# Optimization experiments

Measured on AMD Instinct MI355X. Metric: run time of the kernel, lower is better.

Reference implementation:

```python
import jax, jax.numpy as jnp
import numpy as np

B = 32768; E = 9; RANK = 50; K = 2
N_ENT = 40943; N_REL = 22
LOSS_COEF = 0.01; NOISE_EPS = 0.01
EPS = float(np.finfo(np.float64).eps)


def setup_inputs():
    key = jax.random.key(0)
    ks = jax.random.split(key, 12)
    q0 = jax.random.randint(ks[0], (B,), 0, N_ENT)
    q1 = jax.random.randint(ks[1], (B,), 0, N_REL)
    q2 = jax.random.randint(ks[2], (B,), 0, N_ENT)
    queries = jnp.stack([q0, q1, q2], axis=1)
    t2 = jax.random.randint(ks[3], (B,), 0, N_ENT)
    these_queries = jnp.stack([q0, q1, t2], axis=1)
    D = E * RANK
    entity = jax.random.normal(ks[4], (N_ENT, D), jnp.float32) / D
    rel = jax.random.normal(ks[5], (N_REL, 2 * D), jnp.float32) / (2 * D)
    rel_diag = 2.0 * jax.random.uniform(ks[6], (N_REL, D), jnp.float32) - 1.0
    bh = jnp.zeros((N_ENT, 1), jnp.float32)
    bt = jnp.zeros((N_ENT, 1), jnp.float32)
    c_param = jnp.ones((N_REL, 1), jnp.float32)
    cnn_w = 0.1 * jax.random.normal(ks[7], (1, 1, 5, 5), jnp.float32)
    cnn_b = jnp.zeros((1,), jnp.float32)
    h2e_w = 0.05 * jax.random.normal(ks[8], (E, 128), jnp.float32)
    h2e_b = jnp.zeros((E,), jnp.float32)
    cnnn_w = 0.1 * jax.random.normal(ks[9], (1, 1, 5, 5), jnp.float32)
    cnnn_b = jnp.zeros((1,), jnp.float32)
    h2en_w = 0.05 * jax.random.normal(ks[10], (E, 128), jnp.float32)
    h2en_b = jnp.zeros((E,), jnp.float32)
    noise = jax.random.normal(ks[11], (B, E), jnp.float32)
    return {"queries": queries, "these_queries": these_queries, "entity": entity,
            "rel": rel, "rel_diag": rel_diag, "bh": bh, "bt": bt, "c_param": c_param,
            "cnn_w": cnn_w, "cnn_b": cnn_b, "h2e_w": h2e_w, "h2e_b": h2e_b,
            "cnnn_w": cnnn_w, "cnnn_b": cnnn_b, "h2en_w": h2en_w, "h2en_b": h2en_b,
            "noise": noise}


def _conv(x, w, b):
    # x: [B,1,27,50], w: [1,1,5,5], stride 3, VALID -> [B,1,8,16]
    y = jax.lax.conv_general_dilated(x, w, (3, 3), 'VALID',
                                     dimension_numbers=('NCHW', 'OIHW', 'NCHW'))
    return y + b.reshape(1, -1, 1, 1)


def _phi(z):
    # standard normal CDF
    return 0.5 * (1.0 + jax.lax.erf(z * 0.7071067811865476))


def _givens_rot(r, x):
    # r, x: [B,E,RANK]; rotate consecutive dim-pairs by normalized (cos,sin) from r
    shp = r.shape[:-1] + (RANK // 2, 2)
    r2 = r.reshape(shp); x2 = x.reshape(shp)
    nrm = jnp.maximum(jnp.linalg.norm(r2, axis=-1, keepdims=True), 1e-15)
    cs = r2 / nrm
    o0 = cs[..., 0] * x2[..., 0] - cs[..., 1] * x2[..., 1]
    o1 = cs[..., 1] * x2[..., 0] + cs[..., 0] * x2[..., 1]
    return jnp.stack([o0, o1], axis=-1).reshape(r.shape)


def _cv_squared(v):
    return jnp.var(v, ddof=1) / (jnp.mean(v) ** 2 + 1e-10)


def reference(queries, these_queries, entity, rel, rel_diag, bh, bt, c_param,
              cnn_w, cnn_b, h2e_w, h2e_b, cnnn_w, cnnn_b, h2en_w, h2en_b, noise):
    q0, q1 = queries[:, 0], queries[:, 1]
    t2 = these_queries[:, 2]
    head = entity[q0]                  # [B, E*RANK]
    rel_q = rel[q1]                    # [B, 2*E*RANK]
    rel_diag_q = rel_diag[q1]          # [B, E*RANK]
    c = jax.nn.softplus(c_param[q1])   # [B, 1]
    lhs_b = bh[q0]                     # [B, 1]
    rhs_b = bt[t2]                     # [B, 1]
    rhs_e = entity[t2]                 # [B, E*RANK]

    # ---- noisy top-k gating ----
    x = jnp.concatenate([head, rel_q], axis=-1).reshape(-1, 1, 3 * E, RANK)
    feat = _conv(x, cnn_w, cnn_b).reshape(-1, 128)
    clean = feat @ h2e_w.T + h2e_b                      # [B, E]
    feat_n = _conv(x, cnnn_w, cnnn_b).reshape(-1, 128)
    raw_std = feat_n @ h2en_w.T + h2en_b
    std = jax.nn.softplus(raw_std) + NOISE_EPS
    noisy = clean + noise * std                         # train=1

    top_logits, top_idx = jax.lax.top_k(noisy, K + 1)
    tk_logits = top_logits[:, :K]
    tk_idx = top_idx[:, :K]
    tk_gates = jax.nn.softmax(tk_logits, axis=-1)
    gates = jnp.zeros_like(noisy).at[jnp.arange(noisy.shape[0])[:, None], tk_idx].set(tk_gates)

    thr_in = top_logits[:, K:K + 1]
    thr_out = top_logits[:, K - 1:K]
    is_in = noisy > thr_in
    prob = jnp.where(is_in, _phi((clean - thr_in) / std), _phi((clean - thr_out) / std))
    load = prob.sum(0)
    importance = gates.sum(0)
    loss = LOSS_COEF * (_cv_squared(importance) + _cv_squared(load))

    # ---- experts, computed densely over [B, E, RANK] then masked-combined ----
    head_r = head.reshape(-1, E, RANK)
    rhs_r = rhs_e.reshape(-1, E, RANK)
    rel_r = rel_q.reshape(-1, E, 2 * RANK)
    rd_r = rel_diag_q.reshape(-1, E, RANK)
    lhs = _givens_rot(rd_r, head_r) + rel_r[..., :RANK]
    dist2 = jnp.sum((lhs - rhs_r) ** 2, axis=-1)        # [B, E]
    score = lhs_b + rhs_b - c * dist2                   # [B, E]

    # SparseDispatcher.combine with use_log_sum_exp=True, multiply_by_gates=False
    mask = gates > 0
    s = jnp.sum(jnp.where(mask, jnp.exp(score), 0.0), axis=1, keepdims=True)
    y = jnp.log(jnp.where(s == 0, EPS, s))              # [B, 1]
    return y, loss
```

## Files before the change

### kernel.cpp

```cpp
#include <hip/hip_runtime.h>
#include <math.h>

#define BATCH 32768
#define NE 9
#define RANK 50
#define DIM 450
#define REL_DIM 900
#define N_REL 22
#define EPSV 2.2204460492503131e-16f

__device__ __forceinline__ float softplusf(float x) {
    return (x > 20.f) ? x : log1pf(expf(x));
}
__device__ __forceinline__ float phif(float z) {
    return 0.5f * (1.f + erff(z * 0.70710678118654752f));
}

__global__ __launch_bounds__(64) void k_pre(
    const float* __restrict__ rel, const float* __restrict__ rel_diag,
    const float* __restrict__ c_param,
    const float* __restrict__ cnn_w, const float* __restrict__ cnn_b,
    const float* __restrict__ cnnn_w, const float* __restrict__ cnnn_b,
    const float* __restrict__ h2e_w, const float* __restrict__ h2en_w,
    float* __restrict__ cs_tab, float* __restrict__ pre_out, float* __restrict__ c_soft,
    int* __restrict__ counter)
{
    const int r = blockIdx.x;
    const int l = threadIdx.x;
    __shared__ float rl[REL_DIM];
    __shared__ float fA[80], fB[80];

    const float* relp = rel + (size_t)r * REL_DIM;
    for (int i = l; i < REL_DIM; i += 64) rl[i] = relp[i];
    __syncthreads();

    const float cb0 = cnn_b[0], cb1 = cnnn_b[0];
    for (int idx = l; idx < 80; idx += 64) {
        int o = 48 + idx;
        int oh = o >> 4, ow = o & 15;
        const float* base = rl + (oh * 3 - 9) * RANK + ow * 3;
        float a0 = cb0, a1 = cb1;
#pragma unroll
        for (int i = 0; i < 5; ++i)
#pragma unroll
            for (int j = 0; j < 5; ++j) {
                float v = base[i * RANK + j];
                a0 = fmaf(v, cnn_w[i * 5 + j], a0);
                a1 = fmaf(v, cnnn_w[i * 5 + j], a1);
            }
        fA[idx] = a0; fB[idx] = a1;
    }
    __syncthreads();

    if (l < 18) {
        int e = (l < 9) ? l : (l - 9);
        const float* w = ((l < 9) ? (h2e_w + e * 128) : (h2en_w + e * 128)) + 48;
        const float* f = (l < 9) ? fA : fB;
        float acc = 0.f;
#pragma unroll 8
        for (int t = 0; t < 80; ++t) acc = fmaf(f[t], w[t], acc);
        pre_out[r * 18 + l] = acc;
    }
    if (l == 63) c_soft[r] = softplusf(c_param[r]);
    if (r == 0 && l == 62) *counter = 0;

    const float2* rd2 = (const float2*)(rel_diag + (size_t)r * DIM);
    float2* cs2 = (float2*)(cs_tab + (size_t)r * DIM);
    for (int u = l; u < 225; u += 64) {
        float2 v = rd2[u];
        float nrm = fmaxf(sqrtf(v.x * v.x + v.y * v.y), 1e-15f);
        cs2[u] = make_float2(v.x / nrm, v.y / nrm);
    }
}

struct WaveShm {
    float  xs[552];
    float2 fs[51];
    float  clean[NE], stdv[NE], noisy[NE];
    float  sg[2], sthr[2];
    int    sidx[2];
    int    pad;
};

__global__ __launch_bounds__(256, 8) void k_main(
    const int* __restrict__ queries, const int* __restrict__ these_queries,
    const float* __restrict__ entity, const float* __restrict__ rel,
    const float* __restrict__ bh, const float* __restrict__ bt,
    const float* __restrict__ cnn_w, const float* __restrict__ cnn_b,
    const float* __restrict__ h2e_w, const float* __restrict__ h2e_b,
    const float* __restrict__ cnnn_w, const float* __restrict__ cnnn_b,
    const float* __restrict__ h2en_w, const float* __restrict__ h2en_b,
    const float* __restrict__ noise,
    const float* __restrict__ cs_tab, const float* __restrict__ pre_out,
    const float* __restrict__ c_soft,
    float* __restrict__ y_out, float* __restrict__ ws_rows)
{
    __shared__ WaveShm shm[4];
    const int w = threadIdx.x >> 6;
    const int l = threadIdx.x & 63;
    const int b = blockIdx.x * 4 + w;
    WaveShm& S = shm[w];

    const int q0 = queries[b * 3 + 0];
    const int q1 = queries[b * 3 + 1];
    const int t2 = these_queries[b * 3 + 2];

    const float2* hp2 = (const float2*)(entity + (size_t)q0 * DIM);
    const float2* rp2 = (const float2*)(rel + (size_t)q1 * REL_DIM);

    float2 h2[4];
#pragma unroll
    for (int k = 0; k < 4; ++k) { int i = l + 64 * k; if (i < 225) h2[k] = hp2[i]; }
    float2 rr2 = make_float2(0.f, 0.f);
    if (l < 50) rr2 = rp2[l];
    float nz = 0.f;
    if (l < NE) nz = noise[(size_t)b * NE + l];
    float pre_v = 0.f;
    if (l < 18) pre_v = pre_out[q1 * 18 + l];

    float2* xs2 = (float2*)S.xs;
#pragma unroll
    for (int k = 0; k < 4; ++k) { int i = l + 64 * k; if (i < 225) xs2[i] = h2[k]; }
    if (l < 50) xs2[225 + l] = rr2;
    __syncthreads();

    if (l < 48) {
        int oh = l >> 4, ow = l & 15;
        const float* base = S.xs + (oh * 3) * RANK + ow * 3;
        float a0 = cnn_b[0], a1 = cnnn_b[0];
#pragma unroll
        for (int i = 0; i < 5; ++i)
#pragma unroll
            for (int j = 0; j < 5; ++j) {
                float v = base[i * RANK + j];
                a0 = fmaf(v, cnn_w[i * 5 + j], a0);
                a1 = fmaf(v, cnnn_w[i * 5 + j], a1);
            }
        S.fs[l + (l >> 4)] = make_float2(a0, a1);
    }
    __syncthreads();

    float acc = 0.f;
    if (l < 54) {
        int chunk = l / 18, j = l - chunk * 18;
        int e = (j < 9) ? j : (j - 9);
        const float* wrow = ((j < 9) ? (h2e_w + e * 128) : (h2en_w + e * 128)) + chunk * 16;
        int fbase = chunk * 17;
        if (j < 9) {
#pragma unroll
            for (int k = 0; k < 16; ++k) acc = fmaf(S.fs[fbase + k].x, wrow[k], acc);
        } else {
#pragma unroll
            for (int k = 0; k < 16; ++k) acc = fmaf(S.fs[fbase + k].y, wrow[k], acc);
        }
    }
    float pA = __shfl_down(acc, 18);
    float pB = __shfl_down(acc, 36);
    float tot = acc + pA + pB;
    if (l < 9)        S.clean[l]     = tot + pre_v + h2e_b[l];
    else if (l < 18)  S.stdv[l - 9]  = softplusf(tot + pre_v + h2en_b[l - 9]) + 0.01f;
    __syncthreads();
    if (l < NE) S.noisy[l] = fmaf(nz, S.stdv[l], S.clean[l]);
    __syncthreads();

    if (l == 0) {
        int i0 = -1, i1 = -1;
        float v0 = -__builtin_huge_valf(), v1 = v0, v2 = v0;
#pragma unroll
        for (int e = 0; e < NE; ++e) {
            float v = S.noisy[e];
            if (v > v0)      { v2 = v1; v1 = v0; i1 = i0; v0 = v; i0 = e; }
            else if (v > v1) { v2 = v1; v1 = v; i1 = e; }
            else if (v > v2) { v2 = v; }
        }
        float e1 = expf(v1 - v0);
        float inv = 1.f / (1.f + e1);
        S.sidx[0] = i0; S.sidx[1] = i1;
        S.sg[0] = inv; S.sg[1] = e1 * inv;
        S.sthr[0] = v2; S.sthr[1] = v1;
    }
    __syncthreads();

    float contrib = 0.f;
    bool act = (l < 25) || (l >= 32 && l < 57);
    if (act) {
        int sel = (l >= 32) ? 1 : 0;
        int p = l - 32 * sel;
        int e = S.sidx[sel];
        int u = e * 25 + p;
        float2 cs = *(const float2*)(cs_tab + (size_t)q1 * DIM + 2 * u);
        float2 rl = *(const float2*)(rel + (size_t)q1 * REL_DIM + e * 100 + 2 * p);
        float2 rh = *(const float2*)(entity + (size_t)t2 * DIM + 2 * u);
        float2 x  = xs2[u];
        float o0 = cs.x * x.x - cs.y * x.y + rl.x;
        float o1 = cs.y * x.x + cs.x * x.y + rl.y;
        float d0 = o0 - rh.x, d1 = o1 - rh.y;
        contrib = fmaf(d0, d0, d1 * d1);
    }

    if (l < NE) {
        float g = (l == S.sidx[0]) ? S.sg[0] : ((l == S.sidx[1]) ? S.sg[1] : 0.f);
        ws_rows[(size_t)b * 18 + l] = g;
    } else if (l < 18) {
        int e = l - 9;
        float thr_in = S.sthr[0], thr_out = S.sthr[1];
        float n = S.noisy[e];
        float thr = (n > thr_in) ? thr_in : thr_out;
        ws_rows[(size_t)b * 18 + 9 + e] = phif((S.clean[e] - thr) / S.stdv[e]);
    }

#pragma unroll
    for (int off = 16; off; off >>= 1) contrib += __shfl_xor(contrib, off);
    float d2b = __shfl(contrib, 32);
    if (l == 0) {
        float c = c_soft[q1];
        float base = bh[q0] + bt[t2];
        float s = expf(base - c * contrib) + expf(base - c * d2b);
        y_out[b] = logf((s == 0.f) ? EPSV : s);
    }
}

__global__ __launch_bounds__(64) void k_reduce(const float* __restrict__ ws_rows,
                                               float* __restrict__ partials,
                                               int* __restrict__ counter,
                                               float* __restrict__ out)
{
    const int blk = blockIdx.x, t = threadIdx.x;
    float acc[18];
#pragma unroll
    for (int j = 0; j < 18; ++j) acc[j] = 0.f;
    const int r0 = blk * 128 + t * 2;
#pragma unroll
    for (int rr = 0; rr < 2; ++rr) {
        const float2* row = (const float2*)(ws_rows + (size_t)(r0 + rr) * 18);
#pragma unroll
        for (int j = 0; j < 9; ++j) {
            float2 v = row[j];
            acc[2 * j] += v.x; acc[2 * j + 1] += v.y;
        }
    }
#pragma unroll
    for (int j = 0; j < 18; ++j) {
        float v = acc[j];
        for (int off = 32; off; off >>= 1) v += __shfl_down(v, off);
        if (t == 0) partials[blk * 18 + j] = v;
    }

    __shared__ int is_last;
    __threadfence();
    if (t == 0) {
        int old = atomicAdd(counter, 1);
        is_last = (old == 255) ? 1 : 0;
    }
    __syncthreads();
    if (!is_last) return;
    __threadfence();

    __shared__ float sums[18];
    if (t < 18) {
        float s = 0.f;
        for (int p = 0; p < 256; ++p) s += partials[p * 18 + t];
        sums[t] = s;
    }
    __syncthreads();
    if (t == 0) {
        float loss = 0.f;
#pragma unroll
        for (int part = 0; part < 2; ++part) {
            const float* v = sums + part * NE;
            float mean = 0.f;
            for (int i = 0; i < NE; ++i) mean += v[i];
            mean /= 9.f;
            float var = 0.f;
            for (int i = 0; i < NE; ++i) { float d = v[i] - mean; var += d * d; }
            var /= 8.f;
            loss += var / (mean * mean + 1e-10f);
        }
        out[BATCH] = 0.01f * loss;
    }
}

extern "C" void kernel_launch(void* const* d_in, const int* in_sizes, int n_in,
                              void* d_out, int out_size, void* d_ws, size_t ws_size,
                              hipStream_t stream)
{
    const int*   queries = (const int*)d_in[0];
    const int*   these   = (const int*)d_in[1];
    const float* entity  = (const float*)d_in[2];
    const float* rel     = (const float*)d_in[3];
    const float* rel_dg  = (const float*)d_in[4];
    const float* bh      = (const float*)d_in[5];
    const float* bt      = (const float*)d_in[6];
    const float* c_par   = (const float*)d_in[7];
    const float* cnn_w   = (const float*)d_in[8];
    const float* cnn_b   = (const float*)d_in[9];
    const float* h2e_w   = (const float*)d_in[10];
    const float* h2e_b   = (const float*)d_in[11];
    const float* cnnn_w  = (const float*)d_in[12];
    const float* cnnn_b  = (const float*)d_in[13];
    const float* h2en_w  = (const float*)d_in[14];
    const float* h2en_b  = (const float*)d_in[15];
    const float* noise   = (const float*)d_in[16];

    float* y  = (float*)d_out;
    float* ws = (float*)d_ws;
    float* ws_rows  = ws;
    float* partials = ws + (size_t)BATCH * 18;
    float* cs_tab   = partials + 256 * 18;
    float* pre_out  = cs_tab + N_REL * DIM;
    float* c_soft   = pre_out + N_REL * 18;
    int*   counter  = (int*)(c_soft + N_REL);

    k_pre<<<N_REL, 64, 0, stream>>>(rel, rel_dg, c_par, cnn_w, cnn_b, cnnn_w, cnnn_b,
                                    h2e_w, h2en_w, cs_tab, pre_out, c_soft, counter);
    k_main<<<BATCH / 4, 256, 0, stream>>>(queries, these, entity, rel, bh, bt,
                                          cnn_w, cnn_b, h2e_w, h2e_b, cnnn_w, cnnn_b,
                                          h2en_w, h2en_b, noise, cs_tab, pre_out, c_soft,
                                          y, ws_rows);
    k_reduce<<<256, 64, 0, stream>>>(ws_rows, partials, counter, y);
}
```

Measured before the change: 199.5 us.

## Fuse load-balancing reduction into main kernel with per-wave loop over samples

Removes the separate reduce kernel and the per-row gates and load workspace writes. Each block is now a single wave that handles four samples in sequence. It keeps the h2e weights in registers, accumulates the gate and load statistics locally, then issues one atomicAdd per block into global sums, and the last block computes the loss. This cuts global memory traffic and a kernel launch. In exchange it adds per-sample block barriers, serial dependency inside each wave, and 8192 blocks contending on the same 18 atomic addresses plus the counter.

```diff
diff --git a/kernel.cpp b/kernel.cpp
--- a/kernel.cpp
+++ b/kernel.cpp
@@ -2,6 +2,8 @@
 #include <math.h>
 
 #define BATCH 32768
+#define SPW 4
+#define NBLK (BATCH / SPW)
 #define NE 9
 #define RANK 50
 #define DIM 450
@@ -23,7 +25,7 @@
     const float* __restrict__ cnnn_w, const float* __restrict__ cnnn_b,
     const float* __restrict__ h2e_w, const float* __restrict__ h2en_w,
     float* __restrict__ cs_tab, float* __restrict__ pre_out, float* __restrict__ c_soft,
-    int* __restrict__ counter)
+    float* __restrict__ gsums, int* __restrict__ counter)
 {
     const int r = blockIdx.x;
     const int l = threadIdx.x;
@@ -62,7 +64,10 @@
         pre_out[r * 18 + l] = acc;
     }
     if (l == 63) c_soft[r] = softplusf(c_param[r]);
-    if (r == 0 && l == 62) *counter = 0;
+    if (r == 0) {
+        if (l >= 32 && l < 50) gsums[l - 32] = 0.f;
+        if (l == 62) *counter = 0;
+    }
 
     const float2* rd2 = (const float2*)(rel_diag + (size_t)r * DIM);
     float2* cs2 = (float2*)(cs_tab + (size_t)r * DIM);
@@ -79,10 +84,9 @@
     float  clean[NE], stdv[NE], noisy[NE];
     float  sg[2], sthr[2];
     int    sidx[2];
-    int    pad;
 };
 
-__global__ __launch_bounds__(256, 8) void k_main(
+__global__ __launch_bounds__(64) void k_main(
     const int* __restrict__ queries, const int* __restrict__ these_queries,
     const float* __restrict__ entity, const float* __restrict__ rel,
     const float* __restrict__ bh, const float* __restrict__ bt,
@@ -93,181 +97,165 @@
     const float* __restrict__ noise,
     const float* __restrict__ cs_tab, const float* __restrict__ pre_out,
     const float* __restrict__ c_soft,
-    float* __restrict__ y_out, float* __restrict__ ws_rows)
+    float* __restrict__ y_out, float* __restrict__ gsums, int* __restrict__ counter)
 {
-    __shared__ WaveShm shm[4];
-    const int w = threadIdx.x >> 6;
-    const int l = threadIdx.x & 63;
-    const int b = blockIdx.x * 4 + w;
-    WaveShm& S = shm[w];
-
-    const int q0 = queries[b * 3 + 0];
-    const int q1 = queries[b * 3 + 1];
-    const int t2 = these_queries[b * 3 + 2];
-
-    const float2* hp2 = (const float2*)(entity + (size_t)q0 * DIM);
-    const float2* rp2 = (const float2*)(rel + (size_t)q1 * REL_DIM);
-
-    float2 h2[4];
-#pragma unroll
-    for (int k = 0; k < 4; ++k) { int i = l + 64 * k; if (i < 225) h2[k] = hp2[i]; }
-    float2 rr2 = make_float2(0.f, 0.f);
-    if (l < 50) rr2 = rp2[l];
-    float nz = 0.f;
-    if (l < NE) nz = noise[(size_t)b * NE + l];
-    float pre_v = 0.f;
-    if (l < 18) pre_v = pre_out[q1 * 18 + l];
-
+    __shared__ WaveShm S;
+    const int l = threadIdx.x;
     float2* xs2 = (float2*)S.xs;
-#pragma unroll
-    for (int k = 0; k < 4; ++k) { int i = l + 64 * k; if (i < 225) xs2[i] = h2[k]; }
-    if (l < 50) xs2[225 + l] = rr2;
-    __syncthreads();
-
-    if (l < 48) {
-        int oh = l >> 4, ow = l & 15;
-        const float* base = S.xs + (oh * 3) * RANK + ow * 3;
-        float a0 = cnn_b[0], a1 = cnnn_b[0];
-#pragma unroll
-        for (int i = 0; i < 5; ++i)
-#pragma unroll
-            for (int j = 0; j < 5; ++j) {
-                float v = base[i * RANK + j];
-                a0 = fmaf(v, cnn_w[i * 5 + j], a0);
-                a1 = fmaf(v, cnnn_w[i * 5 + j], a1);
+
+    const int chunk = l / 18, j18 = l - chunk * 18;
+    float wreg[16];
+    if (l < 54) {
+        int e = (j18 < 9) ? j18 : (j18 - 9);
+        const float* wrow = ((j18 < 9) ? (h2e_w + e * 128) : (h2en_w + e * 128)) + chunk * 16;
+#pragma unroll
+        for (int k = 0; k < 16; ++k) wreg[k] = wrow[k];
+    } else {
+#pragma unroll
+        for (int k = 0; k < 16; ++k) wreg[k] = 0.f;
+    }
+    const float cb0 = cnn_b[0], cb1 = cnnn_b[0];
+    float bias18 = 0.f;
+    if (l < 9)            bias18 = h2e_b[l];
+    else if (l < 18)      bias18 = h2en_b[l - 9];
+
+    float accum = 0.f;
+
+    for (int s = 0; s < SPW; ++s) {
+        const int b = blockIdx.x * SPW + s;
+
+        const int q0 = queries[b * 3 + 0];
+        const int q1 = queries[b * 3 + 1];
+        const int t2 = these_queries[b * 3 + 2];
+
+        const float2* hp2 = (const float2*)(entity + (size_t)q0 * DIM);
+        const float2* rp2 = (const float2*)(rel + (size_t)q1 * REL_DIM);
+
+        float2 h2[4];
+#pragma unroll
+        for (int k = 0; k < 4; ++k) { int i = l + 64 * k; if (i < 225) h2[k] = hp2[i]; }
+        float2 rr2 = make_float2(0.f, 0.f);
+        if (l < 50) rr2 = rp2[l];
+        float nz = 0.f;
+        if (l < NE) nz = noise[(size_t)b * NE + l];
+        float pre_v = 0.f;
+        if (l < 18) pre_v = pre_out[q1 * 18 + l];
+
+        __syncthreads();
+#pragma unroll
+        for (int k = 0; k < 4; ++k) { int i = l + 64 * k; if (i < 225) xs2[i] = h2[k]; }
+        if (l < 50) xs2[225 + l] = rr2;
+        __syncthreads();
+
+        if (l < 48) {
+            int oh = l >> 4, ow = l & 15;
+            const float* base = S.xs + (oh * 3) * RANK + ow * 3;
+            float a0 = cb0, a1 = cb1;
+#pragma unroll
+            for (int i = 0; i < 5; ++i)
+#pragma unroll
+                for (int j = 0; j < 5; ++j) {
+                    float v = base[i * RANK + j];
+                    a0 = fmaf(v, cnn_w[i * 5 + j], a0);
+                    a1 = fmaf(v, cnnn_w[i * 5 + j], a1);
+                }
+            S.fs[l + (l >> 4)] = make_float2(a0, a1);
+        }
+        __syncthreads();
+
+        float acc = 0.f;
+        if (l < 54) {
+            int fbase = chunk * 17;
+            if (j18 < 9) {
+#pragma unroll
+                for (int k = 0; k < 16; ++k) acc = fmaf(S.fs[fbase + k].x, wreg[k], acc);
+            } else {
+#pragma unroll
+                for (int k = 0; k < 16; ++k) acc = fmaf(S.fs[fbase + k].y, wreg[k], acc);
             }
-        S.fs[l + (l >> 4)] = make_float2(a0, a1);
-    }
-    __syncthreads();
-
-    float acc = 0.f;
-    if (l < 54) {
-        int chunk = l / 18, j = l - chunk * 18;
-        int e = (j < 9) ? j : (j - 9);
-        const float* wrow = ((j < 9) ? (h2e_w + e * 128) : (h2en_w + e * 128)) + chunk * 16;
-        int fbase = chunk * 17;
-        if (j < 9) {
-#pragma unroll
-            for (int k = 0; k < 16; ++k) acc = fmaf(S.fs[fbase + k].x, wrow[k], acc);
-        } else {
-#pragma unroll
-            for (int k = 0; k < 16; ++k) acc = fmaf(S.fs[fbase + k].y, wrow[k], acc);
-        }
-    }
-    float pA = __shfl_down(acc, 18);
-    float pB = __shfl_down(acc, 36);
-    float tot = acc + pA + pB;
-    if (l < 9)        S.clean[l]     = tot + pre_v + h2e_b[l];
-    else if (l < 18)  S.stdv[l - 9]  = softplusf(tot + pre_v + h2en_b[l - 9]) + 0.01f;
-    __syncthreads();
-    if (l < NE) S.noisy[l] = fmaf(nz, S.stdv[l], S.clean[l]);
-    __syncthreads();
-
-    if (l == 0) {
-        int i0 = -1, i1 = -1;
-        float v0 = -__builtin_huge_valf(), v1 = v0, v2 = v0;
-#pragma unroll
-        for (int e = 0; e < NE; ++e) {
-            float v = S.noisy[e];
-            if (v > v0)      { v2 = v1; v1 = v0; i1 = i0; v0 = v; i0 = e; }
-            else if (v > v1) { v2 = v1; v1 = v; i1 = e; }
-            else if (v > v2) { v2 = v; }
-        }
-        float e1 = expf(v1 - v0);
-        float inv = 1.f / (1.f + e1);
-        S.sidx[0] = i0; S.sidx[1] = i1;
-        S.sg[0] = inv; S.sg[1] = e1 * inv;
-        S.sthr[0] = v2; S.sthr[1] = v1;
-    }
-    __syncthreads();
-
-    float contrib = 0.f;
-    bool act = (l < 25) || (l >= 32 && l < 57);
-    if (act) {
-        int sel = (l >= 32) ? 1 : 0;
-        int p = l - 32 * sel;
-        int e = S.sidx[sel];
-        int u = e * 25 + p;
-        float2 cs = *(const float2*)(cs_tab + (size_t)q1 * DIM + 2 * u);
-        float2 rl = *(const float2*)(rel + (size_t)q1 * REL_DIM + e * 100 + 2 * p);
-        float2 rh = *(const float2*)(entity + (size_t)t2 * DIM + 2 * u);
-        float2 x  = xs2[u];
-        float o0 = cs.x * x.x - cs.y * x.y + rl.x;
-        float o1 = cs.y * x.x + cs.x * x.y + rl.y;
-        float d0 = o0 - rh.x, d1 = o1 - rh.y;
-        contrib = fmaf(d0, d0, d1 * d1);
-    }
-
-    if (l < NE) {
-        float g = (l == S.sidx[0]) ? S.sg[0] : ((l == S.sidx[1]) ? S.sg[1] : 0.f);
-        ws_rows[(size_t)b * 18 + l] = g;
-    } else if (l < 18) {
-        int e = l - 9;
-        float thr_in = S.sthr[0], thr_out = S.sthr[1];
-        float n = S.noisy[e];
-        float thr = (n > thr_in) ? thr_in : thr_out;
-        ws_rows[(size_t)b * 18 + 9 + e] = phif((S.clean[e] - thr) / S.stdv[e]);
-    }
-
-#pragma unroll
-    for (int off = 16; off; off >>= 1) contrib += __shfl_xor(contrib, off);
-    float d2b = __shfl(contrib, 32);
-    if (l == 0) {
-        float c = c_soft[q1];
-        float base = bh[q0] + bt[t2];
-        float s = expf(base - c * contrib) + expf(base - c * d2b);
-        y_out[b] = logf((s == 0.f) ? EPSV : s);
-    }
-}
-
-__global__ __launch_bounds__(64) void k_reduce(const float* __restrict__ ws_rows,
-                                               float* __restrict__ partials,
-                                               int* __restrict__ counter,
-                                               float* __restrict__ out)
-{
-    const int blk = blockIdx.x, t = threadIdx.x;
-    float acc[18];
-#pragma unroll
-    for (int j = 0; j < 18; ++j) acc[j] = 0.f;
-    const int r0 = blk * 128 + t * 2;
-#pragma unroll
-    for (int rr = 0; rr < 2; ++rr) {
-        const float2* row = (const float2*)(ws_rows + (size_t)(r0 + rr) * 18);
-#pragma unroll
-        for (int j = 0; j < 9; ++j) {
-            float2 v = row[j];
-            acc[2 * j] += v.x; acc[2 * j + 1] += v.y;
-        }
-    }
-#pragma unroll
-    for (int j = 0; j < 18; ++j) {
-        float v = acc[j];
-        for (int off = 32; off; off >>= 1) v += __shfl_down(v, off);
-        if (t == 0) partials[blk * 18 + j] = v;
-    }
+        }
+        float pA = __shfl_down(acc, 18);
+        float pB = __shfl_down(acc, 36);
+        float tot = acc + pA + pB;
+        if (l < 9)        S.clean[l]     = tot + pre_v + bias18;
+        else if (l < 18)  S.stdv[l - 9]  = softplusf(tot + pre_v + bias18) + 0.01f;
+        __syncthreads();
+        if (l < NE) S.noisy[l] = fmaf(nz, S.stdv[l], S.clean[l]);
+        __syncthreads();
+
+        if (l == 0) {
+            int i0 = -1, i1 = -1;
+            float v0 = -__builtin_huge_valf(), v1 = v0, v2 = v0;
+#pragma unroll
+            for (int e = 0; e < NE; ++e) {
+                float v = S.noisy[e];
+                if (v > v0)      { v2 = v1; v1 = v0; i1 = i0; v0 = v; i0 = e; }
+                else if (v > v1) { v2 = v1; v1 = v; i1 = e; }
+                else if (v > v2) { v2 = v; }
+            }
+            float e1 = expf(v1 - v0);
+            float inv = 1.f / (1.f + e1);
+            S.sidx[0] = i0; S.sidx[1] = i1;
+            S.sg[0] = inv; S.sg[1] = e1 * inv;
+            S.sthr[0] = v2; S.sthr[1] = v1;
+        }
+        __syncthreads();
+
+        float contrib = 0.f;
+        bool act = (l < 25) || (l >= 32 && l < 57);
+        if (act) {
+            int sel = (l >= 32) ? 1 : 0;
+            int p = l - 32 * sel;
+            int e = S.sidx[sel];
+            int u = e * 25 + p;
+            float2 cs = *(const float2*)(cs_tab + (size_t)q1 * DIM + 2 * u);
+            float2 rl = *(const float2*)(rel + (size_t)q1 * REL_DIM + e * 100 + 2 * p);
+            float2 rh = *(const float2*)(entity + (size_t)t2 * DIM + 2 * u);
+            float2 x  = xs2[u];
+            float o0 = cs.x * x.x - cs.y * x.y + rl.x;
+            float o1 = cs.y * x.x + cs.x * x.y + rl.y;
+            float d0 = o0 - rh.x, d1 = o1 - rh.y;
+            contrib = fmaf(d0, d0, d1 * d1);
+        }
+
+        if (l < NE) {
+            float g = (l == S.sidx[0]) ? S.sg[0] : ((l == S.sidx[1]) ? S.sg[1] : 0.f);
+            accum += g;
+        } else if (l < 18) {
+            int e = l - 9;
+            float thr_in = S.sthr[0], thr_out = S.sthr[1];
+            float n = S.noisy[e];
+            float thr = (n > thr_in) ? thr_in : thr_out;
+            accum += phif((S.clean[e] - thr) / S.stdv[e]);
+        }
+
+#pragma unroll
+        for (int off = 16; off; off >>= 1) contrib += __shfl_xor(contrib, off);
+        float d2b = __shfl(contrib, 32);
+        if (l == 0) {
+            float c = c_soft[q1];
+            float base = bh[q0] + bt[t2];
+            float sum = expf(base - c * contrib) + expf(base - c * d2b);
+            y_out[b] = logf((sum == 0.f) ? EPSV : sum);
+        }
+    }
+
+    if (l < 18) atomicAdd(&gsums[l], accum);
 
     __shared__ int is_last;
     __threadfence();
-    if (t == 0) {
-        int old = atomicAdd(counter, 1);
-        is_last = (old == 255) ? 1 : 0;
-    }
+    if (l == 0) is_last = (atomicAdd(counter, 1) == NBLK - 1) ? 1 : 0;
     __syncthreads();
     if (!is_last) return;
     __threadfence();
 
-    __shared__ float sums[18];
-    if (t < 18) {
-        float s = 0.f;
-        for (int p = 0; p < 256; ++p) s += partials[p * 18 + t];
-        sums[t] = s;
-    }
-    __syncthreads();
-    if (t == 0) {
+    if (l == 0) {
+        volatile float* vs = (volatile float*)gsums;
         float loss = 0.f;
 #pragma unroll
         for (int part = 0; part < 2; ++part) {
-            const float* v = sums + part * NE;
+            float v[NE];
+            for (int i = 0; i < NE; ++i) v[i] = vs[part * NE + i];
             float mean = 0.f;
             for (int i = 0; i < NE; ++i) mean += v[i];
             mean /= 9.f;
@@ -276,7 +264,7 @@
             var /= 8.f;
             loss += var / (mean * mean + 1e-10f);
         }
-        out[BATCH] = 0.01f * loss;
+        y_out[BATCH] = 0.01f * loss;
     }
 }
 
@@ -304,18 +292,16 @@
 
     float* y  = (float*)d_out;
     float* ws = (float*)d_ws;
-    float* ws_rows  = ws;
-    float* partials = ws + (size_t)BATCH * 18;
-    float* cs_tab   = partials + 256 * 18;
-    float* pre_out  = cs_tab + N_REL * DIM;
-    float* c_soft   = pre_out + N_REL * 18;
-    int*   counter  = (int*)(c_soft + N_REL);
+    float* cs_tab  = ws;
+    float* pre_out = cs_tab + N_REL * DIM;
+    float* c_soft  = pre_out + N_REL * 18;
+    float* gsums   = c_soft + N_REL;
+    int*   counter = (int*)(gsums + 18);
 
     k_pre<<<N_REL, 64, 0, stream>>>(rel, rel_dg, c_par, cnn_w, cnn_b, cnnn_w, cnnn_b,
-                                    h2e_w, h2en_w, cs_tab, pre_out, c_soft, counter);
-    k_main<<<BATCH / 4, 256, 0, stream>>>(queries, these, entity, rel, bh, bt,
-                                          cnn_w, cnn_b, h2e_w, h2e_b, cnnn_w, cnnn_b,
-                                          h2en_w, h2en_b, noise, cs_tab, pre_out, c_soft,
-                                          y, ws_rows);
-    k_reduce<<<256, 64, 0, stream>>>(ws_rows, partials, counter, y);
-}
+                                    h2e_w, h2en_w, cs_tab, pre_out, c_soft, gsums, counter);
+    k_main<<<NBLK, 64, 0, stream>>>(queries, these, entity, rel, bh, bt,
+                                    cnn_w, cnn_b, h2e_w, h2e_b, cnnn_w, cnnn_b,
+                                    h2en_w, h2en_b, noise, cs_tab, pre_out, c_soft,
+                                    y, gsums, counter);
+}
```

New measurement: 357.2 us. +79.1%, slower.
